# Kernel tuning notes

Measured on AMD Instinct MI355X. Metric: run time of the kernel, lower is better.

Reference implementation:

```python
import jax, jax.numpy as jnp
import numpy as np

# Standard JPEG luminance quantization table (quality 50)
_QTABLE = np.array([
    [16, 11, 10, 16, 24, 40, 51, 61],
    [12, 12, 14, 19, 26, 58, 60, 55],
    [14, 13, 16, 24, 40, 57, 69, 56],
    [14, 17, 22, 29, 51, 87, 80, 62],
    [18, 22, 37, 56, 68, 109, 103, 77],
    [24, 35, 55, 64, 81, 104, 113, 92],
    [49, 64, 78, 87, 103, 121, 120, 101],
    [72, 92, 95, 98, 112, 100, 103, 99]], dtype=np.float32)

def _dct_mtx(n=8):
    # Orthonormal DCT-II basis matrix: mtx @ block @ mtx.T is the 2-D DCT,
    # so mtx.T @ coeffs @ mtx is the inverse DCT used by this module.
    k = np.arange(n)[:, None]
    j = np.arange(n)[None, :]
    m = np.cos(np.pi * (2 * j + 1) * k / (2 * n)) * np.sqrt(2.0 / n)
    m[0, :] /= np.sqrt(2.0)
    return m.astype(np.float32)

def setup_inputs() -> dict:
    key = jax.random.key(0)
    B, C, H, W = 32, 1, 1024, 1024  # square image required by the reshape chain
    x = jax.random.normal(key, (B, C, H, W), dtype=jnp.float32) * 10.0
    return {
        "x": x,
        "qtable": jnp.asarray(_QTABLE),
        "mtx": jnp.asarray(_dct_mtx(8)),
    }

def reference(x, qtable, mtx):
    B, D1, D2, D3 = x.shape
    # view -> permute -> reshape chain extracting 8x8 blocks (faithful to torch code)
    y = x.reshape(B, D1 * D2 // 8, 8, D3)
    y = jnp.transpose(y, (0, 1, 3, 2))                       # (B, D1*D2/8, D3, 8)
    y = y.reshape(B, D1 * D2 * D3 // 64, 8, 8)
    y = jnp.transpose(y, (0, 1, 3, 2))                       # (B, Nblk, 8, 8)
    y = y * qtable                                           # dequantize
    # mtx.T @ y @ mtx  (batched tiny 8x8 IDCT)
    y = jnp.einsum('ji,bnjk,kl->bnil', mtx, y, mtx)
    # inverse reshape/permute chain back to image layout
    y = jnp.transpose(y, (0, 1, 3, 2))
    y = y.reshape(B, D1 * D2 // 8, D2, 8)
    y = jnp.transpose(y, (0, 1, 3, 2))
    return y.reshape(x.shape) + 128.0
```

## Files before the change

### kernel.cpp

```cpp
#include <hip/hip_runtime.h>


__global__ __launch_bounds__(256) void bidct_kernel(
    const float* __restrict__ x, const float* __restrict__ qt,
    const float* __restrict__ mtx, float* __restrict__ out)
{
    __shared__ float sM[64];
    __shared__ float sQ[64];
    const int t = threadIdx.x;
    if (t < 64) { sM[t] = mtx[t]; sQ[t] = qt[t]; }
    __syncthreads();

    const int n = blockIdx.x * 256 + t;
    const int base = ((n >> 7) << 13) + ((n & 127) << 3);

    float X[8][8];
#pragma unroll
    for (int j = 0; j < 8; ++j) {
        const float4* p = reinterpret_cast<const float4*>(x + base + j * 1024);
        float4 a = p[0];
        float4 b = p[1];
        X[j][0] = a.x; X[j][1] = a.y; X[j][2] = a.z; X[j][3] = a.w;
        X[j][4] = b.x; X[j][5] = b.y; X[j][6] = b.z; X[j][7] = b.w;
    }
#pragma unroll
    for (int j = 0; j < 8; ++j)
#pragma unroll
        for (int k = 0; k < 8; ++k)
            X[j][k] *= sQ[j * 8 + k];

    float T[8][8];
#pragma unroll
    for (int i = 0; i < 8; ++i) {
#pragma unroll
        for (int k = 0; k < 8; ++k) {
            float acc = 0.0f;
#pragma unroll
            for (int j = 0; j < 8; ++j)
                acc += sM[j * 8 + i] * X[j][k];
            T[i][k] = acc;
        }
    }

#pragma unroll
    for (int i = 0; i < 8; ++i) {
        float o[8];
#pragma unroll
        for (int l = 0; l < 8; ++l) {
            float acc = 128.0f;
#pragma unroll
            for (int k = 0; k < 8; ++k)
                acc += T[i][k] * sM[k * 8 + l];
            o[l] = acc;
        }
        float4* q = reinterpret_cast<float4*>(out + base + i * 1024);
        q[0] = make_float4(o[0], o[1], o[2], o[3]);
        q[1] = make_float4(o[4], o[5], o[6], o[7]);
    }
}

extern "C" void kernel_launch(void* const* d_in, const int* in_sizes, int n_in,
                              void* d_out, int out_size, void* d_ws, size_t ws_size,
                              hipStream_t stream) {
    const float* x    = (const float*)d_in[0];
    const float* qt   = (const float*)d_in[1];
    const float* mtx  = (const float*)d_in[2];
    float*       out  = (float*)d_out;

    const int total_blocks = out_size / 64;
    const int grid = (total_blocks + 255) / 256;
    bidct_kernel<<<grid, 256, 0, stream>>>(x, qt, mtx, out);
}
```

Measured before the change: 235.1 us.

## Stage 8x8 blocks through shared memory and split each block across eight threads

```diff
diff --git a/kernel.cpp b/kernel.cpp
--- a/kernel.cpp
+++ b/kernel.cpp
@@ -1,73 +1,95 @@
 #include <hip/hip_runtime.h>
 
 
-__global__ __launch_bounds__(256) void bidct_kernel(
+__global__ __launch_bounds__(256, 8) void bidct_kernel(
     const float* __restrict__ x, const float* __restrict__ qt,
     const float* __restrict__ mtx, float* __restrict__ out)
 {
+    __shared__ float tile[2048];
     __shared__ float sM[64];
     __shared__ float sQ[64];
+
     const int t = threadIdx.x;
     if (t < 64) { sM[t] = mtx[t]; sQ[t] = qt[t]; }
     __syncthreads();
 
-    const int n = blockIdx.x * 256 + t;
-    const int base = ((n >> 7) << 13) + ((n & 127) << 3);
+    const int w = blockIdx.x;
+    const int base = (w >> 2) * 8192 + (w & 3) * 256;
 
-    float X[8][8];
+    float4* tile4 = reinterpret_cast<float4*>(tile);
+    const float4* sM4 = reinterpret_cast<const float4*>(sM);
+
+#pragma unroll
+    for (int r = 0; r < 2; ++r) {
+        const int f  = r * 256 + t;
+        const int j  = f >> 6;
+        const int c4 = f & 63;
+        float4 v = *reinterpret_cast<const float4*>(x + base + j * 1024 + c4 * 4);
+        const int k0 = (c4 & 1) * 4;
+        v.x *= sQ[j * 8 + k0 + 0];
+        v.y *= sQ[j * 8 + k0 + 1];
+        v.z *= sQ[j * 8 + k0 + 2];
+        v.w *= sQ[j * 8 + k0 + 3];
+        tile4[f] = v;
+    }
+    __syncthreads();
+
+    const int bl = t >> 3;
+    const int i  = t & 7;
+
+    float T[8] = {0.f, 0.f, 0.f, 0.f, 0.f, 0.f, 0.f, 0.f};
 #pragma unroll
     for (int j = 0; j < 8; ++j) {
-        const float4* p = reinterpret_cast<const float4*>(x + base + j * 1024);
-        float4 a = p[0];
-        float4 b = p[1];
-        X[j][0] = a.x; X[j][1] = a.y; X[j][2] = a.z; X[j][3] = a.w;
-        X[j][4] = b.x; X[j][5] = b.y; X[j][6] = b.z; X[j][7] = b.w;
-    }
-#pragma unroll
-    for (int j = 0; j < 8; ++j)
-#pragma unroll
-        for (int k = 0; k < 8; ++k)
-            X[j][k] *= sQ[j * 8 + k];
-
-    float T[8][8];
-#pragma unroll
-    for (int i = 0; i < 8; ++i) {
-#pragma unroll
-        for (int k = 0; k < 8; ++k) {
-            float acc = 0.0f;
-#pragma unroll
-            for (int j = 0; j < 8; ++j)
-                acc += sM[j * 8 + i] * X[j][k];
-            T[i][k] = acc;
-        }
+        const float m = sM[j * 8 + i];
+        const float4 xa = tile4[j * 64 + bl * 2];
+        const float4 xb = tile4[j * 64 + bl * 2 + 1];
+        T[0] = fmaf(m, xa.x, T[0]);
+        T[1] = fmaf(m, xa.y, T[1]);
+        T[2] = fmaf(m, xa.z, T[2]);
+        T[3] = fmaf(m, xa.w, T[3]);
+        T[4] = fmaf(m, xb.x, T[4]);
+        T[5] = fmaf(m, xb.y, T[5]);
+        T[6] = fmaf(m, xb.z, T[6]);
+        T[7] = fmaf(m, xb.w, T[7]);
     }
 
+    float o[8] = {128.f, 128.f, 128.f, 128.f, 128.f, 128.f, 128.f, 128.f};
 #pragma unroll
-    for (int i = 0; i < 8; ++i) {
-        float o[8];
+    for (int k = 0; k < 8; ++k) {
+        const float4 m0 = sM4[k * 2];
+        const float4 m1 = sM4[k * 2 + 1];
+        o[0] = fmaf(T[k], m0.x, o[0]);
+        o[1] = fmaf(T[k], m0.y, o[1]);
+        o[2] = fmaf(T[k], m0.z, o[2]);
+        o[3] = fmaf(T[k], m0.w, o[3]);
+        o[4] = fmaf(T[k], m1.x, o[4]);
+        o[5] = fmaf(T[k], m1.y, o[5]);
+        o[6] = fmaf(T[k], m1.z, o[6]);
+        o[7] = fmaf(T[k], m1.w, o[7]);
+    }
+    __syncthreads();
+
+    tile4[i * 64 + bl * 2]     = make_float4(o[0], o[1], o[2], o[3]);
+    tile4[i * 64 + bl * 2 + 1] = make_float4(o[4], o[5], o[6], o[7]);
+    __syncthreads();
+
 #pragma unroll
-        for (int l = 0; l < 8; ++l) {
-            float acc = 128.0f;
-#pragma unroll
-            for (int k = 0; k < 8; ++k)
-                acc += T[i][k] * sM[k * 8 + l];
-            o[l] = acc;
-        }
-        float4* q = reinterpret_cast<float4*>(out + base + i * 1024);
-        q[0] = make_float4(o[0], o[1], o[2], o[3]);
-        q[1] = make_float4(o[4], o[5], o[6], o[7]);
+    for (int r = 0; r < 2; ++r) {
+        const int f  = r * 256 + t;
+        const int j  = f >> 6;
+        const int c4 = f & 63;
+        *reinterpret_cast<float4*>(out + base + j * 1024 + c4 * 4) = tile4[f];
     }
 }
 
 extern "C" void kernel_launch(void* const* d_in, const int* in_sizes, int n_in,
                               void* d_out, int out_size, void* d_ws, size_t ws_size,
                               hipStream_t stream) {
-    const float* x    = (const float*)d_in[0];
-    const float* qt   = (const float*)d_in[1];
-    const float* mtx  = (const float*)d_in[2];
-    float*       out  = (float*)d_out;
+    const float* x   = (const float*)d_in[0];
+    const float* qt  = (const float*)d_in[1];
+    const float* mtx = (const float*)d_in[2];
+    float*       out = (float*)d_out;
 
-    const int total_blocks = out_size / 64;
-    const int grid = (total_blocks + 255) / 256;
+    const int grid = out_size / 2048;
     bidct_kernel<<<grid, 256, 0, stream>>>(x, qt, mtx, out);
 }
```

Result: faster. 230.3 us (-2.0%).
